# Performance work log

Measured on AMD Instinct MI355X. Metric: run time of the kernel, lower is better.

## Reference

```python
import jax, jax.numpy as jnp
import numpy as np

D_IN = 1024
D_OUT = 1024
N_HEADS = 16

def setup_inputs() -> dict:
    key = jax.random.key(0)
    ks = jax.random.split(key, 6)
    s = 0.02
    return {
        "x": jax.random.normal(ks[0], (4, 2048, D_IN), dtype=jnp.float32),
        "Wq": jax.random.normal(ks[1], (D_IN, D_OUT), dtype=jnp.float32) * s,
        "Wk": jax.random.normal(ks[2], (D_IN, D_OUT), dtype=jnp.float32) * s,
        "Wv": jax.random.normal(ks[3], (D_IN, D_OUT), dtype=jnp.float32) * s,
        "Wo": jax.random.normal(ks[4], (D_OUT, D_OUT), dtype=jnp.float32) * s,
        "bo": jax.random.normal(ks[5], (D_OUT,), dtype=jnp.float32) * s,
    }

def reference(x, Wq, Wk, Wv, Wo, bo):
    b, n, _ = x.shape
    hd = D_OUT // N_HEADS
    # project and split heads -> [b, h, n, hd]
    def split(t):
        return t.reshape(b, n, N_HEADS, hd).transpose(0, 2, 1, 3)
    q = split(x @ Wq)
    k = split(x @ Wk)
    v = split(x @ Wv)
    scores = jnp.einsum('bhqd,bhkd->bhqk', q, k)  # [b,h,n,n]
    causal = jnp.tril(jnp.ones((n, n), dtype=bool))
    scores = jnp.where(causal, scores, -jnp.inf)
    attn = jax.nn.softmax(scores / jnp.sqrt(jnp.float32(hd)), axis=-1)
    ctx = jnp.einsum('bhqk,bhkd->bhqd', attn, v)  # [b,h,n,hd]
    ctx = ctx.transpose(0, 2, 1, 3).reshape(b, n, D_OUT)
    return ctx @ Wo + bo
```

## Files before the change

kernel.cpp:

```cpp
#include <hip/hip_runtime.h>
#include <stdint.h>

typedef unsigned short u16;
typedef __attribute__((ext_vector_type(8))) short frag8;
typedef __attribute__((ext_vector_type(4))) float f32x4;
typedef __attribute__((ext_vector_type(4))) unsigned short u16x4;
typedef __attribute__((ext_vector_type(2))) unsigned int u32x2;

#define MFMA_BF16(a,b,c) __builtin_amdgcn_mfma_f32_16x16x32_bf16((a),(b),(c),0,0,0)
#define SMSCALE 0.18033688011112042f
#define EXP2R(x) __builtin_amdgcn_exp2f(x)

__device__ __forceinline__ u16 f2bf(float f) {
  union { float f; uint32_t u; } c; c.f = f;
  uint32_t u = c.u;
  uint32_t r = (u + 0x7fffu + ((u >> 16) & 1u)) >> 16;
  return (u16)r;
}

__device__ __forceinline__ uint32_t pack_bf16(float a, float b) {
  uint32_t au = __float_as_uint(a) + 0x8000u;
  uint32_t bu = __float_as_uint(b) + 0x8000u;
  return __builtin_amdgcn_perm(bu, au, 0x07060302u);
}
__device__ __forceinline__ uint32_t pack_bf16_trunc(float a, float b) {
  return __builtin_amdgcn_perm(__float_as_uint(b), __float_as_uint(a), 0x07060302u);
}

__device__ __forceinline__ void async16(const void* g, void* l) {
  __builtin_amdgcn_global_load_lds((const __attribute__((address_space(1))) void*)g,
                                   (__attribute__((address_space(3))) void*)l,
                                   16, 0, 0);
}

__global__ __launch_bounds__(256) void k_convert_x(const float4* __restrict__ x,
                                                   u16* __restrict__ xb) {
  int i = blockIdx.x * 256 + threadIdx.x;
  float4 v = x[i];
  u16x4 o;
  o.x = f2bf(v.x); o.y = f2bf(v.y); o.z = f2bf(v.z); o.w = f2bf(v.w);
  *(u16x4*)(xb + (size_t)i * 4) = o;
}

__global__ __launch_bounds__(256) void k_transpose_w4(
    const float* __restrict__ W0, const float* __restrict__ W1,
    const float* __restrict__ W2, const float* __restrict__ W3,
    u16* __restrict__ D0, u16* __restrict__ D1,
    u16* __restrict__ D2, u16* __restrict__ D3) {
  __shared__ float tile[64][65];
  const int z = blockIdx.z;
  const float* src = (z == 0) ? W0 : (z == 1) ? W1 : (z == 2) ? W2 : W3;
  u16* dst = (z == 0) ? D0 : (z == 1) ? D1 : (z == 2) ? D2 : D3;
  const int bx = blockIdx.x * 64;
  const int by = blockIdx.y * 64;
  const int t = threadIdx.x;
  const int tc = (t & 15) * 4;
  const int tr = t >> 4;
  #pragma unroll
  for (int p = 0; p < 4; ++p) {
    int r = tr + p * 16;
    float4 v = *(const float4*)(src + (size_t)(bx + r) * 1024 + by + tc);
    tile[r][tc + 0] = v.x; tile[r][tc + 1] = v.y;
    tile[r][tc + 2] = v.z; tile[r][tc + 3] = v.w;
  }
  __syncthreads();
  #pragma unroll
  for (int p = 0; p < 4; ++p) {
    int r = tr + p * 16;
    u16x4 o;
    o.x = f2bf(tile[tc + 0][r]);
    o.y = f2bf(tile[tc + 1][r]);
    o.z = f2bf(tile[tc + 2][r]);
    o.w = f2bf(tile[tc + 3][r]);
    *(u16x4*)(dst + (size_t)(by + r) * 1024 + bx + tc) = o;
  }
}

__global__ __launch_bounds__(256, 2) void k_gemm_qkv(const u16* __restrict__ xb,
    const u16* __restrict__ Wqt, const u16* __restrict__ Wkt, const u16* __restrict__ Wvt,
    u16* __restrict__ Qg, u16* __restrict__ Kg, u16* __restrict__ Vtg) {
  __shared__ __attribute__((aligned(16))) u16 smem[4 * 128 * 64];
  u16* T = smem;
  const int m0 = blockIdx.x * 128, n0 = blockIdx.y * 128;
  const int t = threadIdx.x, lane = t & 63, wv = t >> 6;
  const int lm = lane & 15, quad = lane >> 4;
  const int wr = wv >> 1, wc = wv & 1;
  f32x4 acc[3][4][4] = {};

  for (int k0 = 0; k0 < 1024; k0 += 64) {
    #pragma unroll
    for (int it = 0; it < 4; ++it) {
      int chunk = it * 256 + t;
      int r = chunk >> 3;
      int sc = ((chunk & 7) ^ (r & 7)) * 8;
      async16(xb + (size_t)(m0 + r) * 1024 + k0 + sc,
              smem + (size_t)(it * 256 + wv * 64) * 8);
    }
    #pragma unroll
    for (int z = 0; z < 3; ++z) {
      const u16* Bt = (z == 0) ? Wqt : (z == 1) ? Wkt : Wvt;
      #pragma unroll
      for (int it = 0; it < 4; ++it) {
        int chunk = it * 256 + t;
        int r = chunk >> 3;
        int sc = ((chunk & 7) ^ (r & 7)) * 8;
        async16(Bt + (size_t)(n0 + r) * 1024 + k0 + sc,
                smem + (size_t)((z + 1) * 1024 + it * 256 + wv * 64) * 8);
      }
    }
    __syncthreads();
    #pragma unroll
    for (int kk = 0; kk < 2; ++kk) {
      frag8 a[4];
      #pragma unroll
      for (int i = 0; i < 4; ++i) {
        int row = wr * 64 + i * 16 + lm;
        a[i] = *(const frag8*)(smem + row * 64 + (((kk * 4 + quad) ^ (row & 7)) * 8));
      }
      #pragma unroll
      for (int z = 0; z < 3; ++z) {
        #pragma unroll
        for (int j = 0; j < 4; ++j) {
          int row = wc * 64 + j * 16 + lm;
          frag8 b = *(const frag8*)(smem + (z + 1) * 8192 + row * 64 +
                                    (((kk * 4 + quad) ^ (row & 7)) * 8));
          #pragma unroll
          for (int i = 0; i < 4; ++i)
            acc[z][i][j] = MFMA_BF16(a[i], b, acc[z][i][j]);
        }
      }
    }
    __syncthreads();
  }

  #pragma unroll
  for (int z = 0; z < 2; ++z) {
    u16* tgt = z ? Kg : Qg;
    const float sc = z ? 1.0f : SMSCALE;
    #pragma unroll
    for (int i = 0; i < 4; ++i)
      #pragma unroll
      for (int j = 0; j < 4; ++j) {
        const int col = n0 + wc * 64 + j * 16 + lm;
        const int h = col >> 6, d = col & 63;
        #pragma unroll
        for (int reg = 0; reg < 4; ++reg) {
          const int row = m0 + wr * 64 + i * 16 + quad * 4 + reg;
          const int bb = row >> 11, nn = row & 2047;
          tgt[(((size_t)bb * 16 + h) * 2048 + nn) * 64 + d] = f2bf(acc[z][i][j][reg] * sc);
        }
      }
  }
  {
    const int bb = m0 >> 11, nn0 = m0 & 2047;
    const int h0 = n0 >> 6;
    #pragma unroll
    for (int p = 0; p < 2; ++p) {
      if (wc == p) {
        #pragma unroll
        for (int i = 0; i < 4; ++i)
          #pragma unroll
          for (int j = 0; j < 4; ++j) {
            const int rT = j * 16 + lm;
            #pragma unroll
            for (int reg = 0; reg < 4; ++reg) {
              const int cT = wr * 64 + i * 16 + quad * 4 + reg;
              T[rT * 136 + cT] = f2bf(acc[2][i][j][reg]);
            }
          }
      }
      __syncthreads();
      #pragma unroll
      for (int cc = 0; cc < 4; ++cc) {
        int chunk = cc * 256 + t;
        int r = chunk >> 4, tk = (chunk & 15) * 8;
        frag8 v = *(const frag8*)(T + r * 136 + tk);
        *(frag8*)(Vtg + (((size_t)bb * 16 + h0 + p) * 64 + r) * 2048 + nn0 + tk) = v;
      }
      __syncthreads();
    }
  }
}

__global__ __launch_bounds__(256, 2) void k_attn(const u16* __restrict__ Qg,
                                                 const u16* __restrict__ Kg,
                                                 const u16* __restrict__ Vtg,
                                                 u16* __restrict__ ctx) {
  __shared__ __attribute__((aligned(16))) u16 Ks[2][64 * 64];
  __shared__ __attribute__((aligned(16))) u16 Vts[2][64 * 64];
  __shared__ __attribute__((aligned(16))) u16 Ps[4 * 16 * 72];
  const int bid = blockIdx.x;
  const int ib = bid >> 6;
  const int bh = ((bid >> 3) & 7) * 8 + (bid & 7);
  const int qts[4] = {2 * ib, 2 * ib + 1, 30 - 2 * ib, 31 - 2 * ib};
  const int t = threadIdx.x, lane = t & 63, wv = t >> 6;
  const int lm = lane & 15, quad = lane >> 4;
  const int b = bh >> 4, h = bh & 15;
  u16* const PsW = Ps + wv * (16 * 72);

  frag8 aq[4][2];
  #pragma unroll
  for (int qa = 0; qa < 4; ++qa) {
    const u16* qp = Qg + ((size_t)bh * 2048 + qts[qa] * 64 + wv * 16 + lm) * 64 + quad * 8;
    aq[qa][0] = *(const frag8*)(qp);
    aq[qa][1] = *(const frag8*)(qp + 32);
  }
  f32x4 o[4][4] = {};
  float l[4] = {0.f, 0.f, 0.f, 0.f};
  const int nst = 32 - 2 * ib;

  const u16* ksrc[2]; const u16* vsrc[2];
  #pragma unroll
  for (int it = 0; it < 2; ++it) {
    int chunk = it * 256 + t;
    int r = chunk >> 3, c = chunk & 7;
    int sc = (c ^ (r & 7)) * 8;
    ksrc[it] = Kg  + ((size_t)bh * 2048 + r) * 64 + sc;
    vsrc[it] = Vtg + ((size_t)bh * 64 + r) * 2048 + sc;
  }
  int offs[8];
  #pragma unroll
  for (int x = 0; x < 4; ++x)
    #pragma unroll
    for (int y = 0; y < 2; ++y)
      offs[x * 2 + y] = (x * 16 + lm) * 64 + (((y * 4 + quad) ^ (lm & 7)) * 8);

  auto stage = [&](int kt, int buf) {
    #pragma unroll
    for (int it = 0; it < 2; ++it) {
      async16(ksrc[it] + (size_t)kt * 4096, &Ks[buf][(it * 256 + wv * 64) * 8]);
      async16(vsrc[it] + (size_t)kt * 64,   &Vts[buf][(it * 256 + wv * 64) * 8]);
    }
  };

  stage(0, 0);
  for (int kt0 = 0; kt0 < nst; ++kt0) {
    const int cur = kt0 & 1;
    __syncthreads();
    if (kt0 + 1 < nst) stage(kt0 + 1, cur ^ 1);

    frag8 kf[8];
    #pragma unroll
    for (int i = 0; i < 8; ++i) kf[i] = *(const frag8*)(&Ks[cur][offs[i]]);

    uint32_t pk[4][8];
    #pragma unroll
    for (int qa = 0; qa < 4; ++qa) {
      if (qts[qa] < kt0) continue;
      f32x4 s[4];
      #pragma unroll
      for (int kt = 0; kt < 4; ++kt) {
        f32x4 z = {0.f, 0.f, 0.f, 0.f};
        z = MFMA_BF16(kf[kt * 2 + 0], aq[qa][0], z);
        z = MFMA_BF16(kf[kt * 2 + 1], aq[qa][1], z);
        s[kt] = z;
      }
      if (kt0 == qts[qa]) {
        #pragma unroll
        for (int kt = 0; kt < 4; ++kt)
          #pragma unroll
          for (int rg = 0; rg < 4; ++rg)
            if (kt * 16 + quad * 4 + rg > wv * 16 + lm) s[kt][rg] = -3.0e38f;
      }
      float rs = 0.f;
      #pragma unroll
      for (int kt = 0; kt < 4; ++kt) {
        float p0 = EXP2R(s[kt][0]);
        float p1 = EXP2R(s[kt][1]);
        float p2 = EXP2R(s[kt][2]);
        float p3 = EXP2R(s[kt][3]);
        rs += (p0 + p1) + (p2 + p3);
        pk[qa][kt * 2 + 0] = pack_bf16_trunc(p0, p1);
        pk[qa][kt * 2 + 1] = pack_bf16_trunc(p2, p3);
      }
      l[qa] += rs;
    }

    frag8 vf[8];
    #pragma unroll
    for (int i = 0; i < 8; ++i) vf[i] = *(const frag8*)(&Vts[cur][offs[i]]);

    #pragma unroll
    for (int qa = 0; qa < 4; ++qa) {
      if (qts[qa] < kt0) continue;
      #pragma unroll
      for (int kt = 0; kt < 4; ++kt) {
        u32x2 w; w.x = pk[qa][kt * 2 + 0]; w.y = pk[qa][kt * 2 + 1];
        *(u32x2*)(PsW + lm * 72 + kt * 16 + quad * 4) = w;
      }
      #pragma unroll
      for (int ks = 0; ks < 2; ++ks) {
        frag8 bp = *(const frag8*)(PsW + lm * 72 + ks * 32 + quad * 8);
        #pragma unroll
        for (int dt = 0; dt < 4; ++dt)
          o[qa][dt] = MFMA_BF16(vf[dt * 2 + ks], bp, o[qa][dt]);
      }
    }
  }

  #pragma unroll
  for (int qa = 0; qa < 4; ++qa) {
    float lv = l[qa];
    lv += __shfl_xor(lv, 16);
    lv += __shfl_xor(lv, 32);
    const float inv = 1.0f / lv;
    #pragma unroll
    for (int dt = 0; dt < 4; ++dt) {
      *(uint32_t*)(PsW + lm * 72 + dt * 16 + quad * 4)     = pack_bf16(o[qa][dt][0] * inv, o[qa][dt][1] * inv);
      *(uint32_t*)(PsW + lm * 72 + dt * 16 + quad * 4 + 2) = pack_bf16(o[qa][dt][2] * inv, o[qa][dt][3] * inv);
    }
    const int rr = lane >> 2, cc = (lane & 3) * 8;
    const size_t row = (size_t)b * 2048 + qts[qa] * 64 + wv * 16 + rr;
    #pragma unroll
    for (int half = 0; half < 2; ++half) {
      frag8 vo = *(const frag8*)(PsW + rr * 72 + cc + half * 32);
      *(frag8*)(ctx + row * 1024 + h * 64 + cc + half * 32) = vo;
    }
  }
}

__global__ __launch_bounds__(256) void k_gemm_out(const u16* __restrict__ ctx,
    const u16* __restrict__ Wot, const float* __restrict__ bo, float* __restrict__ out) {
  __shared__ __attribute__((aligned(16))) u16 As[128 * 64];
  __shared__ __attribute__((aligned(16))) u16 Bs[128 * 64];
  const int m0 = blockIdx.x * 128, n0 = blockIdx.y * 128;
  const int t = threadIdx.x, lane = t & 63, wv = t >> 6;
  const int lm = lane & 15, quad = lane >> 4;
  const int wr = wv >> 1, wc = wv & 1;
  f32x4 acc[4][4] = {};
  for (int k0 = 0; k0 < 1024; k0 += 64) {
    #pragma unroll
    for (int it = 0; it < 4; ++it) {
      int chunk = it * 256 + t;
      int r = chunk >> 3;
      int sc = ((chunk & 7) ^ (r & 7)) * 8;
      async16(ctx + (size_t)(m0 + r) * 1024 + k0 + sc, As + (size_t)(it * 256 + wv * 64) * 8);
      async16(Wot + (size_t)(n0 + r) * 1024 + k0 + sc, Bs + (size_t)(it * 256 + wv * 64) * 8);
    }
    __syncthreads();
    #pragma unroll
    for (int kk = 0; kk < 2; ++kk) {
      frag8 a[4];
      #pragma unroll
      for (int i = 0; i < 4; ++i) {
        int row = wr * 64 + i * 16 + lm;
        a[i] = *(const frag8*)(As + row * 64 + (((kk * 4 + quad) ^ (row & 7)) * 8));
      }
      #pragma unroll
      for (int j = 0; j < 4; ++j) {
        int row = wc * 64 + j * 16 + lm;
        frag8 b = *(const frag8*)(Bs + row * 64 + (((kk * 4 + quad) ^ (row & 7)) * 8));
        #pragma unroll
        for (int i = 0; i < 4; ++i)
          acc[i][j] = MFMA_BF16(a[i], b, acc[i][j]);
      }
    }
    __syncthreads();
  }
  #pragma unroll
  for (int i = 0; i < 4; ++i)
    #pragma unroll
    for (int j = 0; j < 4; ++j) {
      const int col = n0 + wc * 64 + j * 16 + lm;
      const float bias = bo[col];
      #pragma unroll
      for (int reg = 0; reg < 4; ++reg) {
        const int row = m0 + wr * 64 + i * 16 + quad * 4 + reg;
        out[(size_t)row * 1024 + col] = acc[i][j][reg] + bias;
      }
    }
}

extern "C" void kernel_launch(void* const* d_in, const int* in_sizes, int n_in,
                              void* d_out, int out_size, void* d_ws, size_t ws_size,
                              hipStream_t stream) {
  const float* x  = (const float*)d_in[0];
  const float* Wq = (const float*)d_in[1];
  const float* Wk = (const float*)d_in[2];
  const float* Wv = (const float*)d_in[3];
  const float* Wo = (const float*)d_in[4];
  const float* bo = (const float*)d_in[5];
  float* out = (float*)d_out;
  char* ws = (char*)d_ws;

  u16* xb   = (u16*)(ws);
  u16* Wqt  = (u16*)(ws + ((size_t)16 << 20));
  u16* Wkt  = (u16*)(ws + ((size_t)18 << 20));
  u16* Wvt  = (u16*)(ws + ((size_t)20 << 20));
  u16* Wot  = (u16*)(ws + ((size_t)22 << 20));
  u16* Qg   = (u16*)(ws + ((size_t)24 << 20));
  u16* Kg   = (u16*)(ws + ((size_t)40 << 20));
  u16* Vtg  = (u16*)(ws + ((size_t)56 << 20));
  u16* ctxb = (u16*)(ws + ((size_t)72 << 20));

  k_convert_x<<<8192, 256, 0, stream>>>((const float4*)x, xb);
  k_transpose_w4<<<dim3(16, 16, 4), 256, 0, stream>>>(Wq, Wk, Wv, Wo, Wqt, Wkt, Wvt, Wot);
  k_gemm_qkv<<<dim3(64, 8), 256, 0, stream>>>(xb, Wqt, Wkt, Wvt, Qg, Kg, Vtg);
  k_attn<<<512, 256, 0, stream>>>(Qg, Kg, Vtg, ctxb);
  k_gemm_out<<<dim3(64, 8), 256, 0, stream>>>(ctxb, Wot, bo, out);
}
```

Baseline: 219.5 us.

## Share a 3-stage pipelined 256x128 GEMM core between the QKV and output projections

Both projection GEMMs are rebuilt on one shared core. It uses 512-thread blocks computing 256x128 tiles and a triple-buffered LDS ring, so async global-to-LDS loads for k-step t+2 are issued while MFMAs run on step t. Explicit vmcnt/lgkmcnt waits, split barriers and s_setprio are meant to overlap memory with math instead of stalling at a full barrier every k-step. The QKV kernel now treats the contiguous Wq/Wk/Wv transposes as one 3072-wide matrix over a flat grid, with block IDs remapped across XCDs. The ring needs about 147KB of LDS, which limits each CU to one block and relies on the hand-counted waitcnt logic being correct.

```diff
diff --git a/kernel.cpp b/kernel.cpp
--- a/kernel.cpp
+++ b/kernel.cpp
@@ -76,108 +76,165 @@
   }
 }
 
-__global__ __launch_bounds__(256, 2) void k_gemm_qkv(const u16* __restrict__ xb,
-    const u16* __restrict__ Wqt, const u16* __restrict__ Wkt, const u16* __restrict__ Wvt,
-    u16* __restrict__ Qg, u16* __restrict__ Kg, u16* __restrict__ Vtg) {
-  __shared__ __attribute__((aligned(16))) u16 smem[4 * 128 * 64];
-  u16* T = smem;
-  const int m0 = blockIdx.x * 128, n0 = blockIdx.y * 128;
+__device__ __forceinline__ void gemm_core_256x128(
+    const u16* __restrict__ Ag,
+    const u16* __restrict__ Bg,
+    int m0, int n0, u16* smem, f32x4 (&acc)[4][4]) {
   const int t = threadIdx.x, lane = t & 63, wv = t >> 6;
   const int lm = lane & 15, quad = lane >> 4;
   const int wr = wv >> 1, wc = wv & 1;
-  f32x4 acc[3][4][4] = {};
-
-  for (int k0 = 0; k0 < 1024; k0 += 64) {
-    #pragma unroll
-    for (int it = 0; it < 4; ++it) {
-      int chunk = it * 256 + t;
-      int r = chunk >> 3;
-      int sc = ((chunk & 7) ^ (r & 7)) * 8;
-      async16(xb + (size_t)(m0 + r) * 1024 + k0 + sc,
-              smem + (size_t)(it * 256 + wv * 64) * 8);
-    }
-    #pragma unroll
-    for (int z = 0; z < 3; ++z) {
-      const u16* Bt = (z == 0) ? Wqt : (z == 1) ? Wkt : Wvt;
-      #pragma unroll
-      for (int it = 0; it < 4; ++it) {
-        int chunk = it * 256 + t;
-        int r = chunk >> 3;
-        int sc = ((chunk & 7) ^ (r & 7)) * 8;
-        async16(Bt + (size_t)(n0 + r) * 1024 + k0 + sc,
-                smem + (size_t)((z + 1) * 1024 + it * 256 + wv * 64) * 8);
-      }
-    }
-    __syncthreads();
-    #pragma unroll
-    for (int kk = 0; kk < 2; ++kk) {
-      frag8 a[4];
-      #pragma unroll
-      for (int i = 0; i < 4; ++i) {
-        int row = wr * 64 + i * 16 + lm;
-        a[i] = *(const frag8*)(smem + row * 64 + (((kk * 4 + quad) ^ (row & 7)) * 8));
-      }
-      #pragma unroll
-      for (int z = 0; z < 3; ++z) {
-        #pragma unroll
-        for (int j = 0; j < 4; ++j) {
-          int row = wc * 64 + j * 16 + lm;
-          frag8 b = *(const frag8*)(smem + (z + 1) * 8192 + row * 64 +
-                                    (((kk * 4 + quad) ^ (row & 7)) * 8));
-          #pragma unroll
-          for (int i = 0; i < 4; ++i)
-            acc[z][i][j] = MFMA_BF16(a[i], b, acc[z][i][j]);
-        }
-      }
-    }
-    __syncthreads();
-  }
-
-  #pragma unroll
-  for (int z = 0; z < 2; ++z) {
+
+  const u16* sA[4]; int dA[4];
+  #pragma unroll
+  for (int it = 0; it < 4; ++it) {
+    int chunk = it * 512 + t;
+    int r = chunk >> 3;
+    int sc = ((chunk & 7) ^ (r & 7)) * 8;
+    sA[it] = Ag + (size_t)(m0 + r) * 1024 + sc;
+    dA[it] = (it * 512 + wv * 64) * 8;
+  }
+  const u16* sB[2]; int dB[2];
+  #pragma unroll
+  for (int it = 0; it < 2; ++it) {
+    int chunk = it * 512 + t;
+    int r = chunk >> 3;
+    int sc = ((chunk & 7) ^ (r & 7)) * 8;
+    sB[it] = Bg + (size_t)(n0 + r) * 1024 + sc;
+    dB[it] = 16384 + (it * 512 + wv * 64) * 8;
+  }
+
+  int offA[2][4], offB[2][4];
+  #pragma unroll
+  for (int kk = 0; kk < 2; ++kk) {
+    #pragma unroll
+    for (int i = 0; i < 4; ++i) {
+      int rowa = wr * 64 + i * 16 + lm;
+      offA[kk][i] = rowa * 64 + (((kk * 4 + quad) ^ (rowa & 7)) * 8);
+      int rowb = wc * 64 + i * 16 + lm;
+      offB[kk][i] = 16384 + rowb * 64 + (((kk * 4 + quad) ^ (rowb & 7)) * 8);
+    }
+  }
+
+  #pragma unroll
+  for (int it = 0; it < 4; ++it) async16(sA[it], smem + dA[it]);
+  #pragma unroll
+  for (int it = 0; it < 2; ++it) async16(sB[it], smem + dB[it]);
+  #pragma unroll
+  for (int it = 0; it < 4; ++it) async16(sA[it] + 64, smem + 24576 + dA[it]);
+  #pragma unroll
+  for (int it = 0; it < 2; ++it) async16(sB[it] + 64, smem + 24576 + dB[it]);
+  asm volatile("s_waitcnt vmcnt(6)" ::: "memory");
+  __builtin_amdgcn_s_barrier();
+
+  int cb = 0;
+  for (int tt = 0; tt < 16; ++tt) {
+    u16* base = smem + cb * 24576;
+    int pb = cb + 2; if (pb >= 3) pb -= 3;
+    u16* pbase = smem + pb * 24576;
+    const int kg = (tt + 2) * 64;
+    const bool pf = (tt + 2 < 16);
+    frag8 a[4], b[4];
+
+    #pragma unroll
+    for (int i = 0; i < 4; ++i) a[i] = *(const frag8*)(base + offA[0][i]);
+    #pragma unroll
+    for (int j = 0; j < 4; ++j) b[j] = *(const frag8*)(base + offB[0][j]);
+    if (pf) {
+      async16(sA[0] + kg, pbase + dA[0]);
+      async16(sA[1] + kg, pbase + dA[1]);
+      async16(sB[0] + kg, pbase + dB[0]);
+    }
+    __builtin_amdgcn_s_barrier();
+    asm volatile("s_waitcnt lgkmcnt(0)" ::: "memory");
+    __builtin_amdgcn_s_setprio(1);
+    #pragma unroll
+    for (int j = 0; j < 4; ++j)
+      #pragma unroll
+      for (int i = 0; i < 4; ++i)
+        acc[i][j] = MFMA_BF16(a[i], b[j], acc[i][j]);
+    __builtin_amdgcn_s_setprio(0);
+    __builtin_amdgcn_s_barrier();
+
+    #pragma unroll
+    for (int i = 0; i < 4; ++i) a[i] = *(const frag8*)(base + offA[1][i]);
+    #pragma unroll
+    for (int j = 0; j < 4; ++j) b[j] = *(const frag8*)(base + offB[1][j]);
+    if (pf) {
+      async16(sA[2] + kg, pbase + dA[2]);
+      async16(sA[3] + kg, pbase + dA[3]);
+      async16(sB[1] + kg, pbase + dB[1]);
+    }
+    __builtin_amdgcn_s_barrier();
+    asm volatile("s_waitcnt lgkmcnt(0)" ::: "memory");
+    __builtin_amdgcn_s_setprio(1);
+    #pragma unroll
+    for (int j = 0; j < 4; ++j)
+      #pragma unroll
+      for (int i = 0; i < 4; ++i)
+        acc[i][j] = MFMA_BF16(a[i], b[j], acc[i][j]);
+    __builtin_amdgcn_s_setprio(0);
+    if (pf) { asm volatile("s_waitcnt vmcnt(6)" ::: "memory"); }
+    else    { asm volatile("s_waitcnt vmcnt(0)" ::: "memory"); }
+    __builtin_amdgcn_s_barrier();
+
+    cb = cb + 1; if (cb >= 3) cb = 0;
+  }
+}
+
+__global__ __launch_bounds__(512, 2) void k_gemm_qkv(
+    const u16* __restrict__ xb, const u16* __restrict__ Wt,
+    u16* __restrict__ Qg, u16* __restrict__ Kg, u16* __restrict__ Vtg) {
+  __shared__ __attribute__((aligned(16))) u16 smem[73728];
+  const int bid = blockIdx.x;
+  const int wgid = (bid & 7) * 96 + (bid >> 3);
+  const int mt = wgid / 24, nt_ = wgid - mt * 24;
+  const int m0 = mt * 256, n0 = nt_ * 128;
+  f32x4 acc[4][4] = {};
+  gemm_core_256x128(xb, Wt, m0, n0, smem, acc);
+
+  const int t = threadIdx.x, lane = t & 63, wv = t >> 6;
+  const int lm = lane & 15, quad = lane >> 4;
+  const int wr = wv >> 1, wc = wv & 1;
+  const int z = n0 >> 10, nz = n0 & 1023;
+
+  if (z < 2) {
     u16* tgt = z ? Kg : Qg;
     const float sc = z ? 1.0f : SMSCALE;
     #pragma unroll
     for (int i = 0; i < 4; ++i)
       #pragma unroll
       for (int j = 0; j < 4; ++j) {
-        const int col = n0 + wc * 64 + j * 16 + lm;
+        const int col = nz + wc * 64 + j * 16 + lm;
         const int h = col >> 6, d = col & 63;
         #pragma unroll
         for (int reg = 0; reg < 4; ++reg) {
           const int row = m0 + wr * 64 + i * 16 + quad * 4 + reg;
           const int bb = row >> 11, nn = row & 2047;
-          tgt[(((size_t)bb * 16 + h) * 2048 + nn) * 64 + d] = f2bf(acc[z][i][j][reg] * sc);
+          tgt[(((size_t)bb * 16 + h) * 2048 + nn) * 64 + d] = f2bf(acc[i][j][reg] * sc);
         }
       }
-  }
-  {
-    const int bb = m0 >> 11, nn0 = m0 & 2047;
-    const int h0 = n0 >> 6;
-    #pragma unroll
-    for (int p = 0; p < 2; ++p) {
-      if (wc == p) {
+  } else {
+    u16* T = smem;
+    #pragma unroll
+    for (int i = 0; i < 4; ++i)
+      #pragma unroll
+      for (int j = 0; j < 4; ++j) {
+        const int rT = wc * 64 + j * 16 + lm;
         #pragma unroll
-        for (int i = 0; i < 4; ++i)
-          #pragma unroll
-          for (int j = 0; j < 4; ++j) {
-            const int rT = j * 16 + lm;
-            #pragma unroll
-            for (int reg = 0; reg < 4; ++reg) {
-              const int cT = wr * 64 + i * 16 + quad * 4 + reg;
-              T[rT * 136 + cT] = f2bf(acc[2][i][j][reg]);
-            }
-          }
-      }
-      __syncthreads();
-      #pragma unroll
-      for (int cc = 0; cc < 4; ++cc) {
-        int chunk = cc * 256 + t;
-        int r = chunk >> 4, tk = (chunk & 15) * 8;
-        frag8 v = *(const frag8*)(T + r * 136 + tk);
-        *(frag8*)(Vtg + (((size_t)bb * 16 + h0 + p) * 64 + r) * 2048 + nn0 + tk) = v;
-      }
-      __syncthreads();
+        for (int reg = 0; reg < 4; ++reg) {
+          const int cT = wr * 64 + i * 16 + quad * 4 + reg;
+          T[rT * 264 + cT] = f2bf(acc[i][j][reg]);
+        }
+      }
+    __syncthreads();
+    const int bb = m0 >> 11, nn0 = m0 & 2047, h0 = nz >> 6;
+    #pragma unroll
+    for (int p = 0; p < 8; ++p) {
+      int chunk = p * 512 + t;
+      int r = chunk >> 5, tk = (chunk & 31) * 8;
+      frag8 v = *(const frag8*)(T + r * 264 + tk);
+      *(frag8*)(Vtg + (((size_t)bb * 16 + h0 + (r >> 6)) * 64 + (r & 63)) * 2048 +
+                nn0 + tk) = v;
     }
   }
 }
@@ -319,44 +376,19 @@
   }
 }
 
-__global__ __launch_bounds__(256) void k_gemm_out(const u16* __restrict__ ctx,
-    const u16* __restrict__ Wot, const float* __restrict__ bo, float* __restrict__ out) {
-  __shared__ __attribute__((aligned(16))) u16 As[128 * 64];
-  __shared__ __attribute__((aligned(16))) u16 Bs[128 * 64];
-  const int m0 = blockIdx.x * 128, n0 = blockIdx.y * 128;
+__global__ __launch_bounds__(512, 2) void k_gemm_out(
+    const u16* __restrict__ ctx, const u16* __restrict__ Wot,
+    const float* __restrict__ bo, float* __restrict__ out) {
+  __shared__ __attribute__((aligned(16))) u16 smem[73728];
+  const int bid = blockIdx.x;
+  const int wgid = (bid & 7) * 32 + (bid >> 3);
+  const int m0 = (wgid >> 3) * 256, n0 = (wgid & 7) * 128;
+  f32x4 acc[4][4] = {};
+  gemm_core_256x128(ctx, Wot, m0, n0, smem, acc);
+
   const int t = threadIdx.x, lane = t & 63, wv = t >> 6;
   const int lm = lane & 15, quad = lane >> 4;
   const int wr = wv >> 1, wc = wv & 1;
-  f32x4 acc[4][4] = {};
-  for (int k0 = 0; k0 < 1024; k0 += 64) {
-    #pragma unroll
-    for (int it = 0; it < 4; ++it) {
-      int chunk = it * 256 + t;
-      int r = chunk >> 3;
-      int sc = ((chunk & 7) ^ (r & 7)) * 8;
-      async16(ctx + (size_t)(m0 + r) * 1024 + k0 + sc, As + (size_t)(it * 256 + wv * 64) * 8);
-      async16(Wot + (size_t)(n0 + r) * 1024 + k0 + sc, Bs + (size_t)(it * 256 + wv * 64) * 8);
-    }
-    __syncthreads();
-    #pragma unroll
-    for (int kk = 0; kk < 2; ++kk) {
-      frag8 a[4];
-      #pragma unroll
-      for (int i = 0; i < 4; ++i) {
-        int row = wr * 64 + i * 16 + lm;
-        a[i] = *(const frag8*)(As + row * 64 + (((kk * 4 + quad) ^ (row & 7)) * 8));
-      }
-      #pragma unroll
-      for (int j = 0; j < 4; ++j) {
-        int row = wc * 64 + j * 16 + lm;
-        frag8 b = *(const frag8*)(Bs + row * 64 + (((kk * 4 + quad) ^ (row & 7)) * 8));
-        #pragma unroll
-        for (int i = 0; i < 4; ++i)
-          acc[i][j] = MFMA_BF16(a[i], b, acc[i][j]);
-      }
-    }
-    __syncthreads();
-  }
   #pragma unroll
   for (int i = 0; i < 4; ++i)
     #pragma unroll
@@ -395,7 +427,7 @@
 
   k_convert_x<<<8192, 256, 0, stream>>>((const float4*)x, xb);
   k_transpose_w4<<<dim3(16, 16, 4), 256, 0, stream>>>(Wq, Wk, Wv, Wo, Wqt, Wkt, Wvt, Wot);
-  k_gemm_qkv<<<dim3(64, 8), 256, 0, stream>>>(xb, Wqt, Wkt, Wvt, Qg, Kg, Vtg);
+  k_gemm_qkv<<<768, 512, 0, stream>>>(xb, Wqt, Qg, Kg, Vtg);
   k_attn<<<512, 256, 0, stream>>>(Qg, Kg, Vtg, ctxb);
-  k_gemm_out<<<dim3(64, 8), 256, 0, stream>>>(ctxb, Wot, bo, out);
-}
+  k_gemm_out<<<256, 512, 0, stream>>>(ctxb, Wot, bo, out);
+}
```

New measurement: 244.4 us. 11.4% more time.
